# Optimization experiments

Hardware: AMD Instinct MI355X
Metric: run time of the kernel (lower is better)

Reference implementation:

```python
import jax, jax.numpy as jnp
import numpy as np

B, S, D_MODEL, N_HEADS, D_HEAD = 2, 2048, 512, 8, 64
AMBIENT_K = -1.0
EPS = 1e-7


def log_map_origin(x, K):
    """Lorentz log map at origin, curvature K<0. x: (..., d+1) -> (..., d)."""
    c = -K
    sc = jnp.sqrt(c)
    x_t = x[..., :1]
    x_s = x[..., 1:]
    nrm = jnp.maximum(jnp.linalg.norm(x_s, axis=-1, keepdims=True), EPS)
    theta = jnp.arccosh(jnp.maximum(sc * x_t, 1.0 + EPS)) / sc  # geodesic distance
    return theta * x_s / nrm


def exp_map_batched(u, K_vals):
    """Per-head Lorentz exp map at origin. u: (B,S,H,dh), K_vals: (H,) negative.
    Returns (B,S,H,dh+1) with time component first."""
    c = (-K_vals)[None, None, :, None]          # (1,1,H,1)
    sc = jnp.sqrt(c)
    n = jnp.maximum(jnp.linalg.norm(u, axis=-1, keepdims=True), EPS)
    t = jnp.cosh(sc * n) / sc                   # time component
    s = jnp.sinh(sc * n) / (sc * n) * u         # space components
    return jnp.concatenate([t, s], axis=-1)


def setup_inputs() -> dict:
    key = jax.random.key(0)
    k_x, k_q, k_k, k_v, k_o = jax.random.split(key, 5)
    # Lorentz points on the K=-1 manifold: x_t = sqrt(1 + |x_s|^2)
    x_s = 0.5 * jax.random.normal(k_x, (B, S, D_MODEL), dtype=jnp.float32)
    x_t = jnp.sqrt(1.0 + jnp.sum(x_s * x_s, axis=-1, keepdims=True))
    x = jnp.concatenate([x_t, x_s], axis=-1)    # (B, S, d_model+1)
    scale = 1.0 / np.sqrt(D_MODEL)
    W_q = scale * jax.random.normal(k_q, (D_MODEL, N_HEADS * D_HEAD), dtype=jnp.float32)
    W_k = scale * jax.random.normal(k_k, (D_MODEL, N_HEADS * D_HEAD), dtype=jnp.float32)
    W_v = scale * jax.random.normal(k_v, (D_MODEL, N_HEADS * D_HEAD), dtype=jnp.float32)
    W_o = scale * jax.random.normal(k_o, (N_HEADS * D_HEAD, D_MODEL), dtype=jnp.float32)
    log_abs_K = jnp.zeros((N_HEADS,), dtype=jnp.float32)  # init_K = -1 -> log(1) = 0
    return {"x": x, "W_q": W_q, "W_k": W_k, "W_v": W_v, "W_o": W_o,
            "log_abs_K": log_abs_K}


def reference(x, W_q, W_k, W_v, W_o, log_abs_K):
    b, s, _ = x.shape
    K_vals = -jnp.exp(log_abs_K)                            # (H,) negative curvatures
    x_eu = log_map_origin(x, AMBIENT_K)                     # (B,S,D)
    Q = (x_eu @ W_q).reshape(b, s, N_HEADS, D_HEAD)
    Kp = (x_eu @ W_k).reshape(b, s, N_HEADS, D_HEAD)
    V = (x_eu @ W_v).reshape(b, s, N_HEADS, D_HEAD)
    Q_hyp = exp_map_batched(Q, K_vals).transpose(0, 2, 1, 3)   # (B,H,S,dh+1)
    K_hyp = exp_map_batched(Kp, K_vals).transpose(0, 2, 1, 3)
    V = V.transpose(0, 2, 1, 3)                                # (B,H,S,dh)
    Q_t, Q_s = Q_hyp[..., 0], Q_hyp[..., 1:]
    K_t, K_s = K_hyp[..., 0], K_hyp[..., 1:]
    # Lorentzian inner product: -q_t k_t + <q_s, k_s>
    lorentz_ip = (jnp.einsum('bhqd,bhkd->bhqk', Q_s, K_s)
                  - jnp.einsum('bhq,bhk->bhqk', Q_t, K_t))
    abs_K = jnp.exp(log_abs_K)[None, :, None, None]
    scores = abs_K * (-lorentz_ip) / np.sqrt(D_HEAD)           # (B,H,S,S)
    causal = jnp.triu(jnp.ones((s, s), dtype=bool), k=1)[None, None]
    scores = jnp.where(causal, -jnp.inf, scores)
    attn = jax.nn.softmax(scores, axis=-1)
    out = jnp.einsum('bhqk,bhkd->bhqd', attn, V)               # (B,H,S,dh)
    out = out.transpose(0, 2, 1, 3).reshape(b, s, N_HEADS * D_HEAD)
    return out @ W_o                                           # (B,S,D)
```

## Files before the change

kernel.cpp:

```cpp
#include <hip/hip_runtime.h>
#include <math.h>

#define S_LEN 2048
#define B_SZ 2
#define NH 8
#define DH 64
#define DM 512
#define MROWS 4096

typedef __attribute__((ext_vector_type(8))) short s16x8;
typedef __attribute__((ext_vector_type(4))) float fx4;
typedef __attribute__((ext_vector_type(16))) float fx16;
typedef __attribute__((ext_vector_type(4))) int ix4;

__device__ inline short f2bf(float x){
  unsigned u = __float_as_uint(x);
  u = (u + 0x7FFFu + ((u >> 16) & 1u)) >> 16;
  return (short)u;
}

__device__ inline fx4 mfma16(s16x8 a, s16x8 b, fx4 c){
  return __builtin_amdgcn_mfma_f32_16x16x32_bf16(a, b, c, 0, 0, 0);
}
__device__ inline fx16 mfma32(s16x8 a, s16x8 b, fx16 c){
  return __builtin_amdgcn_mfma_f32_32x32x16_bf16(a, b, c, 0, 0, 0);
}
__device__ inline int cvtpk(float a, float b){
  int r; asm("v_cvt_pk_bf16_f32 %0, %1, %2" : "=v"(r) : "v"(a), "v"(b)); return r;
}

#define GLL16(g, l) __builtin_amdgcn_global_load_lds((const __attribute__((address_space(1))) void*)(g), (__attribute__((address_space(3))) void*)(l), 16, 0, 0)
#define GLL4(g, l)  __builtin_amdgcn_global_load_lds((const __attribute__((address_space(1))) void*)(g), (__attribute__((address_space(3))) void*)(l), 4, 0, 0)

__global__ __launch_bounds__(256) void prep_kernel(const float* __restrict__ W0,
                                                   const float* __restrict__ W1,
                                                   const float* __restrict__ W2,
                                                   const float* __restrict__ W3,
                                                   short* __restrict__ Wt,
                                                   const float* __restrict__ x,
                                                   short* __restrict__ xeu){
  __shared__ short tile[64][66];
  __shared__ float s4[4];
  int bid = blockIdx.x;
  int t = threadIdx.x;
  if (bid < 256){
    int z = bid >> 6, rem = bid & 63;
    const float* W = (z == 0) ? W0 : (z == 1) ? W1 : (z == 2) ? W2 : W3;
    short* Wtz = Wt + (size_t)z * DM * DM;
    int n0 = (rem & 7) * 64, k0 = (rem >> 3) * 64;
    int nl = t & 63;
    #pragma unroll
    for (int p = 0; p < 16; ++p){
      int kl = (t >> 6) + p * 4;
      tile[kl][nl] = f2bf(W[(size_t)(k0 + kl) * DM + n0 + nl]);
    }
    __syncthreads();
    int kl2 = t & 63;
    #pragma unroll
    for (int p = 0; p < 16; ++p){
      int nl2 = (t >> 6) + p * 4;
      Wtz[(size_t)(n0 + nl2) * DM + k0 + kl2] = tile[kl2][nl2];
    }
  } else {
    int row = 2 * (bid - 256) + (t >> 7);
    int tl = t & 127;
    const float* xr = x + (size_t)row * (DM + 1);
    float v[4]; float ss = 0.f;
    #pragma unroll
    for (int j = 0; j < 4; ++j){
      v[j] = xr[1 + tl + 128 * j];
      ss += v[j] * v[j];
    }
    #pragma unroll
    for (int off = 1; off < 64; off <<= 1) ss += __shfl_xor(ss, off);
    if ((t & 63) == 0) s4[t >> 6] = ss;
    __syncthreads();
    int g2 = t >> 7;
    float tot = s4[2 * g2] + s4[2 * g2 + 1];
    float nrm = sqrtf(tot);
    float xt = xr[0];
    float theta = acoshf(fmaxf(xt, 1.0f + 1e-7f));
    float scl = theta / fmaxf(nrm, 1e-7f);
    #pragma unroll
    for (int j = 0; j < 4; ++j)
      xeu[(size_t)row * DM + tl + 128 * j] = f2bf(scl * v[j]);
  }
}

__global__ __launch_bounds__(256, 3) void gemm_fused_kernel(const short* __restrict__ A,
                                                            const short* __restrict__ Bt,
                                                            const float* __restrict__ labsK,
                                                            float* __restrict__ Qt,
                                                            short* __restrict__ Qs,
                                                            float* __restrict__ Kt,
                                                            short* __restrict__ Ks,
                                                            short* __restrict__ Vt){
  __shared__ __attribute__((aligned(16))) short Asm[2][128 * 64];
  __shared__ __attribute__((aligned(16))) short Bsm[2][64 * 64];
  __shared__ float nrm2s[2][128];
  const int K = DM;
  int z = blockIdx.z;
  int h = blockIdx.x;
  int n0 = h * 64, m0 = blockIdx.y * 128;
  int t = threadIdx.x;
  int w = t >> 6, lane = t & 63;
  int wm = w >> 1, wn = w & 1;
  int lg = lane >> 4, lr = lane & 15;
  const short* Btz = Bt + (size_t)z * K * DM;

  int aoff[4]; const short* asrcp[4];
  int boff[2]; const short* bsrcp[2];
  #pragma unroll
  for (int j = 0; j < 4; ++j){
    int ch = t + 256 * j;
    int r = ch >> 3, c = ch & 7;
    aoff[j] = ch * 8;
    asrcp[j] = A + (size_t)(m0 + r) * K + 8 * (c ^ (r & 7));
  }
  #pragma unroll
  for (int j = 0; j < 2; ++j){
    int ch = t + 256 * j;
    int r = ch >> 3, c = ch & 7;
    boff[j] = ch * 8;
    bsrcp[j] = Btz + (size_t)(n0 + r) * K + 8 * (c ^ (r & 7));
  }

  {
    short* ab = &Asm[0][0]; short* bb = &Bsm[0][0];
    #pragma unroll
    for (int j = 0; j < 4; ++j) GLL16(asrcp[j], ab + aoff[j]);
    #pragma unroll
    for (int j = 0; j < 2; ++j) GLL16(bsrcp[j], bb + boff[j]);
  }

  fx4 acc[4][2] = {};
  int buf = 0;
  for (int ks = 0; ks < 8; ++ks){
    if (ks < 7){
      int nb = buf ^ 1;
      short* ab = &Asm[nb][0]; short* bb = &Bsm[nb][0];
      int kk = (ks + 1) * 64;
      #pragma unroll
      for (int j = 0; j < 4; ++j) GLL16(asrcp[j] + kk, ab + aoff[j]);
      #pragma unroll
      for (int j = 0; j < 2; ++j) GLL16(bsrcp[j] + kk, bb + boff[j]);
      asm volatile("s_waitcnt vmcnt(6)" ::: "memory");
    } else {
      asm volatile("s_waitcnt vmcnt(0)" ::: "memory");
    }
    __builtin_amdgcn_s_barrier();

    s16x8 af[4][2], bf[2][2];
    #pragma unroll
    for (int mi = 0; mi < 4; ++mi){
      int row = wm * 64 + mi * 16 + lr;
      #pragma unroll
      for (int s = 0; s < 2; ++s)
        af[mi][s] = *(const s16x8*)&Asm[buf][row * 64 + ((4 * s + lg) ^ (row & 7)) * 8];
    }
    #pragma unroll
    for (int ni = 0; ni < 2; ++ni){
      int row = wn * 32 + ni * 16 + lr;
      #pragma unroll
      for (int s = 0; s < 2; ++s)
        bf[ni][s] = *(const s16x8*)&Bsm[buf][row * 64 + ((4 * s + lg) ^ (row & 7)) * 8];
    }
    #pragma unroll
    for (int s = 0; s < 2; ++s)
      #pragma unroll
      for (int mi = 0; mi < 4; ++mi)
        #pragma unroll
        for (int ni = 0; ni < 2; ++ni)
          acc[mi][ni] = mfma16(af[mi][s], bf[ni][s], acc[mi][ni]);
    __builtin_amdgcn_s_barrier();
    buf ^= 1;
  }

  if (z < 2){
    #pragma unroll
    for (int mi = 0; mi < 4; ++mi)
      #pragma unroll
      for (int r = 0; r < 4; ++r){
        float prt = acc[mi][0][r] * acc[mi][0][r] + acc[mi][1][r] * acc[mi][1][r];
        prt += __shfl_xor(prt, 1);
        prt += __shfl_xor(prt, 2);
        prt += __shfl_xor(prt, 4);
        prt += __shfl_xor(prt, 8);
        if (lr == 0) nrm2s[wn][wm * 64 + mi * 16 + 4 * lg + r] = prt;
      }
    __syncthreads();
    float c  = __expf(labsK[h]);
    float sc = sqrtf(c);
    float invsc = __frcp_rn(sc);
    float a  = 0.125f * c * 1.4426950408889634f;
    float tmul = (z == 0) ? a : 1.0f;
    float vmul = (z == 0) ? -a : 1.0f;
    float* Tt = (z == 0) ? Qt : Kt;
    short* Ts = (z == 0) ? Qs : Ks;
    #pragma unroll
    for (int mi = 0; mi < 4; ++mi)
      #pragma unroll
      for (int r = 0; r < 4; ++r){
        int row_local = wm * 64 + mi * 16 + 4 * lg + r;
        float full = nrm2s[0][row_local] + nrm2s[1][row_local];
        float n = fmaxf(sqrtf(full), 1e-7f);
        float arg = sc * n;
        float e = __expf(arg), ei = __frcp_rn(e);
        float tval = tmul * 0.5f * (e + ei) * invsc;
        float vscl = vmul * 0.5f * (e - ei) * __frcp_rn(arg);
        int grow = m0 + row_local;
        int b = grow >> 11, s = grow & (S_LEN - 1);
        size_t bhs = ((size_t)(b * NH + h) * S_LEN + s);
        if (lr == 0) Tt[bhs] = tval;
        #pragma unroll
        for (int ni = 0; ni < 2; ++ni)
          Ts[bhs * DH + wn * 32 + ni * 16 + lr] = f2bf(vscl * acc[mi][ni][r]);
      }
  } else {
    short* vt = (short*)&Asm[0][0];
    #pragma unroll
    for (int mi = 0; mi < 4; ++mi)
      #pragma unroll
      for (int ni = 0; ni < 2; ++ni)
        #pragma unroll
        for (int r = 0; r < 4; ++r){
          int row_local = wm * 64 + mi * 16 + 4 * lg + r;
          int col_local = wn * 32 + ni * 16 + lr;
          vt[col_local * 136 + row_local] = f2bf(acc[mi][ni][r]);
        }
    __syncthreads();
    int d = t >> 2, sseg = (t & 3) * 32;
    int b = m0 >> 11;
    size_t vbase = ((size_t)(b * NH + h) * DH + d) * S_LEN + (m0 & (S_LEN - 1)) + sseg;
    #pragma unroll
    for (int j = 0; j < 4; ++j){
      s16x8 val = *(const s16x8*)&vt[d * 136 + sseg + 8 * j];
      *(s16x8*)(Vt + vbase + 8 * j) = val;
    }
  }
}

__global__ __launch_bounds__(256, 4) void attn_kernel(const short* __restrict__ Qs,
                                                      const float* __restrict__ Qt,
                                                      const short* __restrict__ Ks,
                                                      const float* __restrict__ Kt,
                                                      const short* __restrict__ Vt,
                                                      float* __restrict__ Mpart,
                                                      float* __restrict__ Lpart,
                                                      float* __restrict__ Opart){
  __shared__ __attribute__((aligned(16))) short Ksm[2][4096];
  __shared__ __attribute__((aligned(16))) short Vsm[2][4096];
  __shared__ __attribute__((aligned(16))) float Ktm[2][64];

  int bx = blockIdx.x;
  int bh = bx & 15;
  int id = bx >> 4;
  int g, c;
  if (id < 4)       { g = id;                 c = 0; }
  else if (id < 12) { g = 4 + ((id - 4) >> 1);  c = (id - 4) & 1; }
  else if (id < 24) { int r = id - 12; int q3 = r / 3; g = 8 + q3; c = r - 3 * q3; }
  else              { g = 12 + ((id - 24) >> 2); c = (id - 24) & 3; }
  int kbeg = 512 * c;
  int kend = 512 * c + 512; { int ge = 128 * g + 128; if (ge < kend) kend = ge; }
  int ntc = (kend - kbeg) >> 6;

  int tid = threadIdx.x;
  int w = tid >> 6, lane = tid & 63;
  int l5 = lane & 31, hi = lane >> 5;
  size_t bhS = (size_t)bh * S_LEN;

  const short* Kg  = Ks + bhS * DH;
  const short* Vg  = Vt + (size_t)bh * DH * S_LEN;
  const float* Ktg = Kt + bhS;

  int srow = lane >> 3;
  int scol = ((lane & 7) * 8) ^ (srow << 3);
  const short* kg0 = Kg + (size_t)(kbeg + 16 * w + srow) * DH + scol;
  const short* kg1 = kg0 + 8 * DH;
  const short* vg0 = Vg + (size_t)(16 * w + srow) * S_LEN + kbeg + scol;
  const short* vg1 = vg0 + 8 * S_LEN;
  const float* ktg = Ktg + kbeg + lane;
  short* Kd0 = &Ksm[0][16 * w * 64]; short* Kd1 = Kd0 + 512;
  short* Vd0 = &Vsm[0][16 * w * 64]; short* Vd1 = Vd0 + 512;

  int q0w = 128 * g + 32 * w;
  int q   = q0w + l5;
  int qmax = q0w + 31;
  s16x8 qf[4];
  #pragma unroll
  for (int dblk = 0; dblk < 4; ++dblk)
    qf[dblk] = *(const s16x8*)(Qs + (bhS + q) * DH + dblk * 16 + hi * 8);
  float aqt = Qt[bhS + q];

  fx16 acc0, acc1;
  #pragma unroll
  for (int i = 0; i < 16; ++i){ acc0[i] = 0.f; acc1[i] = 0.f; }
  float mrun = 0.f, lrun = 0.f;

  GLL16(kg0, Kd0); GLL16(kg1, Kd1);
  GLL16(vg0, Vd0); GLL16(vg1, Vd1);
  if (w == 3) GLL4(ktg, &Ktm[0][0]);
  int buf = 0;

  for (int t = 0; t < ntc; ++t){
    int k0 = kbeg + t * 64;
    if (t + 1 < ntc){
      int off = (t + 1) * 64;
      int bn = buf ^ 1;
      GLL16(kg0 + (size_t)off * DH, &Ksm[bn][16 * w * 64]);
      GLL16(kg1 + (size_t)off * DH, &Ksm[bn][16 * w * 64 + 512]);
      GLL16(vg0 + off, &Vsm[bn][16 * w * 64]);
      GLL16(vg1 + off, &Vsm[bn][16 * w * 64 + 512]);
      if (w == 3){
        GLL4(ktg + off, &Ktm[bn][0]);
        asm volatile("s_waitcnt vmcnt(5)" ::: "memory");
      } else {
        asm volatile("s_waitcnt vmcnt(4)" ::: "memory");
      }
    } else {
      asm volatile("s_waitcnt vmcnt(0)" ::: "memory");
    }
    __builtin_amdgcn_s_barrier();

    if (k0 <= qmax){
      fx16 st[2];
      __builtin_amdgcn_s_setprio(1);
      #pragma unroll
      for (int s = 0; s < 2; ++s){
        const short* kb = &Ksm[buf][(32 * s + l5) * 64];
        fx16 z;
        #pragma unroll
        for (int i = 0; i < 16; ++i) z[i] = 0.f;
        #pragma unroll
        for (int dblk = 0; dblk < 4; ++dblk){
          s16x8 kf = *(const s16x8*)(kb + ((16 * dblk + 8 * hi) ^ ((l5 & 7) << 3)));
          z = mfma32(kf, qf[dblk], z);
        }
        st[s] = z;
      }
      __builtin_amdgcn_s_setprio(0);
      float p[2][16];
      #pragma unroll
      for (int s = 0; s < 2; ++s)
        #pragma unroll
        for (int m4 = 0; m4 < 4; ++m4){
          fx4 kt4 = *(const fx4*)&Ktm[buf][32 * s + 8 * m4 + 4 * hi];
          #pragma unroll
          for (int tt = 0; tt < 4; ++tt)
            p[s][4 * m4 + tt] = st[s][4 * m4 + tt] + aqt * kt4[tt];
        }
      if (k0 + 63 > q0w){
        #pragma unroll
        for (int s = 0; s < 2; ++s)
          #pragma unroll
          for (int r = 0; r < 16; ++r){
            int kg2 = k0 + 32 * s + (r & 3) + 8 * (r >> 2) + 4 * hi;
            if (kg2 > q) p[s][r] = -3e38f;
          }
      }
      float v16[16];
      #pragma unroll
      for (int i = 0; i < 16; ++i) v16[i] = fmaxf(p[0][i], p[1][i]);
      #pragma unroll
      for (int i = 0; i < 8; ++i) v16[i] = fmaxf(v16[i], v16[i + 8]);
      #pragma unroll
      for (int i = 0; i < 4; ++i) v16[i] = fmaxf(v16[i], v16[i + 4]);
      float pmax = fmaxf(fmaxf(v16[0], v16[1]), fmaxf(v16[2], v16[3]));
      pmax = fmaxf(pmax, __shfl_xor(pmax, 32));
      if (!__all(pmax <= mrun + 8.f)){
        float mnew = fmaxf(mrun, pmax);
        float scl = __builtin_amdgcn_exp2f(mrun - mnew);
        mrun = mnew;
        lrun *= scl;
        #pragma unroll
        for (int i = 0; i < 16; ++i){ acc0[i] *= scl; acc1[i] *= scl; }
      }
      float sm[16];
      #pragma unroll
      for (int i = 0; i < 16; ++i){
        p[0][i] = __builtin_amdgcn_exp2f(p[0][i] - mrun);
        p[1][i] = __builtin_amdgcn_exp2f(p[1][i] - mrun);
        sm[i] = p[0][i] + p[1][i];
      }
      #pragma unroll
      for (int i = 0; i < 8; ++i) sm[i] += sm[i + 8];
      #pragma unroll
      for (int i = 0; i < 4; ++i) sm[i] += sm[i + 4];
      float rsum = (sm[0] + sm[1]) + (sm[2] + sm[3]);
      rsum += __shfl_xor(rsum, 32);
      lrun += rsum;

      #pragma unroll
      for (int h = 0; h < 4; ++h){
        int s = h >> 1, hb = h & 1;
        int w0 = cvtpk(p[s][8 * hb + 0], p[s][8 * hb + 1]);
        int w1 = cvtpk(p[s][8 * hb + 2], p[s][8 * hb + 3]);
        int w2 = cvtpk(p[s][8 * hb + 4], p[s][8 * hb + 5]);
        int w3 = cvtpk(p[s][8 * hb + 6], p[s][8 * hb + 7]);
        int sdA = hi ? w0 : w2;
        int sdB = hi ? w1 : w3;
        int rcA = __shfl_xor(sdA, 32);
        int rcB = __shfl_xor(sdB, 32);
        ix4 fw;
        fw.x = hi ? rcA : w0; fw.y = hi ? rcB : w1;
        fw.z = hi ? w2 : rcA; fw.w = hi ? w3 : rcB;
        s16x8 pf = __builtin_bit_cast(s16x8, fw);
        const short* vb0 = &Vsm[buf][(l5) * 64 + ((16 * h + 8 * hi) ^ ((l5 & 7) << 3))];
        const short* vb1 = vb0 + 32 * 64;
        s16x8 vf0 = *(const s16x8*)vb0;
        s16x8 vf1 = *(const s16x8*)vb1;
        __builtin_amdgcn_s_setprio(1);
        acc0 = mfma32(vf0, pf, acc0);
        acc1 = mfma32(vf1, pf, acc1);
        __builtin_amdgcn_s_setprio(0);
      }
    }
    __builtin_amdgcn_s_barrier();
    buf ^= 1;
  }

  int slot = bh * 40 + id;
  if (hi == 0){
    Mpart[(size_t)slot * 128 + 32 * w + l5] = mrun;
    Lpart[(size_t)slot * 128 + 32 * w + l5] = lrun;
  }
  float* Op = Opart + (size_t)slot * 8192 + w * 2048;
  #pragma unroll
  for (int r = 0; r < 16; ++r){
    int d = (r & 3) + 8 * (r >> 2) + 4 * hi;
    Op[d * 32 + l5]        = acc0[r];
    Op[(d + 32) * 32 + l5] = acc1[r];
  }
}

__global__ __launch_bounds__(256) void combine_kernel(const float* __restrict__ Mpart,
                                                      const float* __restrict__ Lpart,
                                                      const float* __restrict__ Opart,
                                                      short* __restrict__ Obf){
  int bx = blockIdx.x;
  int bhg = bx & 255;
  int bh = bhg & 15, g = bhg >> 4;
  int t = threadIdx.x;
  int q = t & 127;
  int dquad = (t >> 7) | ((bx >> 8) << 1);
  int nch = (g >> 2) + 1;
  int pre = (g < 4) ? g : (g < 8 ? 4 + 2 * (g - 4) : (g < 12 ? 12 + 3 * (g - 8) : 24 + 4 * (g - 12)));
  int base = bh * 40 + pre;
  int w = q >> 5, l = q & 31;

  float mc[4], lc[4];
  #pragma unroll
  for (int c = 0; c < 4; ++c){
    mc[c] = Mpart[(size_t)(base + c) * 128 + q];
    lc[c] = Lpart[(size_t)(base + c) * 128 + q];
    if (c >= nch) mc[c] = -3e38f;
  }
  float M = fmaxf(fmaxf(mc[0], mc[1]), fmaxf(mc[2], mc[3]));
  float wc[4]; float L = 0.f;
  #pragma unroll
  for (int c = 0; c < 4; ++c){
    wc[c] = __builtin_amdgcn_exp2f(mc[c] - M);
    L += wc[c] * lc[c];
  }
  float invL = 1.f / L;
  #pragma unroll
  for (int c = 0; c < 4; ++c) wc[c] *= invL;

  const float* ob = Opart + (size_t)base * 8192 + w * 2048 + dquad * 256 + l;
  float f[4][8];
  #pragma unroll
  for (int c = 0; c < 4; ++c)
    #pragma unroll
    for (int dd = 0; dd < 8; ++dd)
      f[c][dd] = ob[(size_t)c * 8192 + dd * 32];
  s16x8 pk;
  #pragma unroll
  for (int dd = 0; dd < 8; ++dd){
    float o = wc[0] * f[0][dd] + wc[1] * f[1][dd] + wc[2] * f[2][dd] + wc[3] * f[3][dd];
    pk[dd] = f2bf(o);
  }
  int bb = bh >> 3, hh = bh & 7;
  *(s16x8*)(Obf + ((size_t)bb * S_LEN + 128 * g + q) * DM + hh * DH + dquad * 8) = pk;
}

__global__ __launch_bounds__(256, 4) void gemm_o_kernel(const short* __restrict__ A,
                                                        const short* __restrict__ Bt,
                                                        float* __restrict__ C){
  __shared__ __attribute__((aligned(16))) short Asm[2][64 * 64];
  __shared__ __attribute__((aligned(16))) short Bsm[2][64 * 64];
  const int K = DM;
  int n0 = blockIdx.x * 64, m0 = blockIdx.y * 64;
  int t = threadIdx.x;
  int w = t >> 6, lane = t & 63;
  int wm = w >> 1, wn = w & 1;
  int lg = lane >> 4, lr = lane & 15;

  int aoff[2]; const short* asrcp[2];
  int boff[2]; const short* bsrcp[2];
  #pragma unroll
  for (int j = 0; j < 2; ++j){
    int ch = t + 256 * j;
    int r = ch >> 3, c = ch & 7;
    aoff[j] = ch * 8;
    asrcp[j] = A + (size_t)(m0 + r) * K + 8 * (c ^ (r & 7));
    boff[j] = ch * 8;
    bsrcp[j] = Bt + (size_t)(n0 + r) * K + 8 * (c ^ (r & 7));
  }

  {
    short* ab = &Asm[0][0]; short* bb = &Bsm[0][0];
    #pragma unroll
    for (int j = 0; j < 2; ++j){ GLL16(asrcp[j], ab + aoff[j]); GLL16(bsrcp[j], bb + boff[j]); }
  }

  fx4 acc[2][2] = {};
  int buf = 0;
  for (int ks = 0; ks < 8; ++ks){
    if (ks < 7){
      int nb = buf ^ 1;
      short* ab = &Asm[nb][0]; short* bb = &Bsm[nb][0];
      int kk = (ks + 1) * 64;
      #pragma unroll
      for (int j = 0; j < 2; ++j){ GLL16(asrcp[j] + kk, ab + aoff[j]); GLL16(bsrcp[j] + kk, bb + boff[j]); }
      asm volatile("s_waitcnt vmcnt(4)" ::: "memory");
    } else {
      asm volatile("s_waitcnt vmcnt(0)" ::: "memory");
    }
    __builtin_amdgcn_s_barrier();

    s16x8 af[2][2], bf[2][2];
    #pragma unroll
    for (int mi = 0; mi < 2; ++mi){
      int row = wm * 32 + mi * 16 + lr;
      #pragma unroll
      for (int s = 0; s < 2; ++s)
        af[mi][s] = *(const s16x8*)&Asm[buf][row * 64 + ((4 * s + lg) ^ (row & 7)) * 8];
    }
    #pragma unroll
    for (int ni = 0; ni < 2; ++ni){
      int row = wn * 32 + ni * 16 + lr;
      #pragma unroll
      for (int s = 0; s < 2; ++s)
        bf[ni][s] = *(const s16x8*)&Bsm[buf][row * 64 + ((4 * s + lg) ^ (row & 7)) * 8];
    }
    #pragma unroll
    for (int s = 0; s < 2; ++s)
      #pragma unroll
      for (int mi = 0; mi < 2; ++mi)
        #pragma unroll
        for (int ni = 0; ni < 2; ++ni)
          acc[mi][ni] = mfma16(af[mi][s], bf[ni][s], acc[mi][ni]);
    __builtin_amdgcn_s_barrier();
    buf ^= 1;
  }

  #pragma unroll
  for (int mi = 0; mi < 2; ++mi)
    #pragma unroll
    for (int ni = 0; ni < 2; ++ni)
      #pragma unroll
      for (int r = 0; r < 4; ++r){
        int row = m0 + wm * 32 + mi * 16 + 4 * lg + r;
        int col = n0 + wn * 32 + ni * 16 + lr;
        C[(size_t)row * DM + col] = acc[mi][ni][r];
      }
}

extern "C" void kernel_launch(void* const* d_in, const int* in_sizes, int n_in,
                              void* d_out, int out_size, void* d_ws, size_t ws_size,
                              hipStream_t stream) {
  const float* x     = (const float*)d_in[0];
  const float* Wq    = (const float*)d_in[1];
  const float* Wk    = (const float*)d_in[2];
  const float* Wv    = (const float*)d_in[3];
  const float* Wo    = (const float*)d_in[4];
  const float* labsK = (const float*)d_in[5];

  char* w = (char*)d_ws;
  short* Wt    = (short*)(w);
  short* xeu   = (short*)(w + (2ull  << 20));
  float* Opart = (float*)(w + (6ull  << 20));
  float* Mpart = (float*)(w + (26ull << 20));
  float* Lpart = (float*)(w + (27ull << 20));
  short* Qs    = (short*)(w + (30ull << 20));
  short* Ks    = (short*)(w + (34ull << 20));
  short* Vt    = (short*)(w + (38ull << 20));
  float* Qt    = (float*)(w + (42ull << 20));
  float* Kt    = (float*)(w + (42ull << 20) + (128ull << 10));
  short* Obf   = (short*)(w + (42ull << 20) + (256ull << 10));

  prep_kernel<<<dim3(2304), 256, 0, stream>>>(Wq, Wk, Wv, Wo, Wt, x, xeu);

  gemm_fused_kernel<<<dim3(8, 32, 3), 256, 0, stream>>>(
      xeu, Wt, labsK, Qt, Qs, Kt, Ks, Vt);

  attn_kernel<<<dim3(640), 256, 0, stream>>>(Qs, Qt, Ks, Kt, Vt, Mpart, Lpart, Opart);

  combine_kernel<<<dim3(1024), 256, 0, stream>>>(Mpart, Lpart, Opart, Obf);

  gemm_o_kernel<<<dim3(8, 64), 256, 0, stream>>>(Obf, Wt + 3 * DM * DM, (float*)d_out);
}
```

Baseline: 66.28 us.

## Fuse split-K combine into attention via atomic counter, triple-buffer K/V, reorder GEMM grids

The separate combine kernel is removed. The last attention block per (bh, query group) detects completion through an atomic counter and performs the split-K softmax merge, writing bf16 output directly. Attention K/V staging becomes triple-buffered with prefetch two tiles ahead, occupancy drops to 3 blocks per SM, and the Opart layout changes to per-query rows for vector stores. The GEMM kernels swap grid axes, move the wait and barrier to the loop top, and raise wave priority around the MFMAs. This adds a memset launch and fence/atomic overhead in exchange for one fewer kernel launch.

```diff
diff --git a/kernel.cpp b/kernel.cpp
--- a/kernel.cpp
+++ b/kernel.cpp
@@ -100,8 +100,8 @@
   __shared__ float nrm2s[2][128];
   const int K = DM;
   int z = blockIdx.z;
-  int h = blockIdx.x;
-  int n0 = h * 64, m0 = blockIdx.y * 128;
+  int h = blockIdx.y;
+  int n0 = h * 64, m0 = blockIdx.x * 128;
   int t = threadIdx.x;
   int w = t >> 6, lane = t & 63;
   int wm = w >> 1, wn = w & 1;
@@ -134,22 +134,19 @@
   }
 
   fx4 acc[4][2] = {};
-  int buf = 0;
   for (int ks = 0; ks < 8; ++ks){
+    asm volatile("s_waitcnt vmcnt(0)" ::: "memory");
+    __builtin_amdgcn_s_barrier();
     if (ks < 7){
-      int nb = buf ^ 1;
+      int nb = (ks + 1) & 1;
       short* ab = &Asm[nb][0]; short* bb = &Bsm[nb][0];
       int kk = (ks + 1) * 64;
       #pragma unroll
       for (int j = 0; j < 4; ++j) GLL16(asrcp[j] + kk, ab + aoff[j]);
       #pragma unroll
       for (int j = 0; j < 2; ++j) GLL16(bsrcp[j] + kk, bb + boff[j]);
-      asm volatile("s_waitcnt vmcnt(6)" ::: "memory");
-    } else {
-      asm volatile("s_waitcnt vmcnt(0)" ::: "memory");
-    }
-    __builtin_amdgcn_s_barrier();
-
+    }
+    int buf = ks & 1;
     s16x8 af[4][2], bf[2][2];
     #pragma unroll
     for (int mi = 0; mi < 4; ++mi){
@@ -165,6 +162,7 @@
       for (int s = 0; s < 2; ++s)
         bf[ni][s] = *(const s16x8*)&Bsm[buf][row * 64 + ((4 * s + lg) ^ (row & 7)) * 8];
     }
+    __builtin_amdgcn_s_setprio(1);
     #pragma unroll
     for (int s = 0; s < 2; ++s)
       #pragma unroll
@@ -172,8 +170,7 @@
         #pragma unroll
         for (int ni = 0; ni < 2; ++ni)
           acc[mi][ni] = mfma16(af[mi][s], bf[ni][s], acc[mi][ni]);
-    __builtin_amdgcn_s_barrier();
-    buf ^= 1;
+    __builtin_amdgcn_s_setprio(0);
   }
 
   if (z < 2){
@@ -218,6 +215,7 @@
       }
   } else {
     short* vt = (short*)&Asm[0][0];
+    __syncthreads();
     #pragma unroll
     for (int mi = 0; mi < 4; ++mi)
       #pragma unroll
@@ -240,17 +238,20 @@
   }
 }
 
-__global__ __launch_bounds__(256, 4) void attn_kernel(const short* __restrict__ Qs,
+__global__ __launch_bounds__(256, 3) void attn_kernel(const short* __restrict__ Qs,
                                                       const float* __restrict__ Qt,
                                                       const short* __restrict__ Ks,
                                                       const float* __restrict__ Kt,
                                                       const short* __restrict__ Vt,
                                                       float* __restrict__ Mpart,
                                                       float* __restrict__ Lpart,
-                                                      float* __restrict__ Opart){
-  __shared__ __attribute__((aligned(16))) short Ksm[2][4096];
-  __shared__ __attribute__((aligned(16))) short Vsm[2][4096];
-  __shared__ __attribute__((aligned(16))) float Ktm[2][64];
+                                                      float* __restrict__ Opart,
+                                                      int* __restrict__ cnt,
+                                                      short* __restrict__ Obf){
+  __shared__ __attribute__((aligned(16))) short Ksm[3][4096];
+  __shared__ __attribute__((aligned(16))) short Vsm[3][4096];
+  __shared__ __attribute__((aligned(16))) float Ktm[3][64];
+  __shared__ int lastFlag;
 
   int bx = blockIdx.x;
   int bh = bx & 15;
@@ -260,6 +261,7 @@
   else if (id < 12) { g = 4 + ((id - 4) >> 1);  c = (id - 4) & 1; }
   else if (id < 24) { int r = id - 12; int q3 = r / 3; g = 8 + q3; c = r - 3 * q3; }
   else              { g = 12 + ((id - 24) >> 2); c = (id - 24) & 3; }
+  int nch = (g >> 2) + 1;
   int kbeg = 512 * c;
   int kend = 512 * c + 512; { int ge = 128 * g + 128; if (ge < kend) kend = ge; }
   int ntc = (kend - kbeg) >> 6;
@@ -280,8 +282,6 @@
   const short* vg0 = Vg + (size_t)(16 * w + srow) * S_LEN + kbeg + scol;
   const short* vg1 = vg0 + 8 * S_LEN;
   const float* ktg = Ktg + kbeg + lane;
-  short* Kd0 = &Ksm[0][16 * w * 64]; short* Kd1 = Kd0 + 512;
-  short* Vd0 = &Vsm[0][16 * w * 64]; short* Vd1 = Vd0 + 512;
 
   int q0w = 128 * g + 32 * w;
   int q   = q0w + l5;
@@ -297,30 +297,27 @@
   for (int i = 0; i < 16; ++i){ acc0[i] = 0.f; acc1[i] = 0.f; }
   float mrun = 0.f, lrun = 0.f;
 
-  GLL16(kg0, Kd0); GLL16(kg1, Kd1);
-  GLL16(vg0, Vd0); GLL16(vg1, Vd1);
-  if (w == 3) GLL4(ktg, &Ktm[0][0]);
-  int buf = 0;
-
+  #define STAGE_T(tt, b) { int off_ = (tt) * 64; \
+    GLL16(kg0 + (size_t)off_ * DH, &Ksm[b][16 * w * 64]); \
+    GLL16(kg1 + (size_t)off_ * DH, &Ksm[b][16 * w * 64 + 512]); \
+    GLL16(vg0 + off_, &Vsm[b][16 * w * 64]); \
+    GLL16(vg1 + off_, &Vsm[b][16 * w * 64 + 512]); \
+    if (w == 3) GLL4(ktg + off_, &Ktm[b][0]); }
+
+  STAGE_T(0, 0);
+  if (ntc > 1) STAGE_T(1, 1);
+
+  int buf = 0, sbuf = 2;
   for (int t = 0; t < ntc; ++t){
     int k0 = kbeg + t * 64;
     if (t + 1 < ntc){
-      int off = (t + 1) * 64;
-      int bn = buf ^ 1;
-      GLL16(kg0 + (size_t)off * DH, &Ksm[bn][16 * w * 64]);
-      GLL16(kg1 + (size_t)off * DH, &Ksm[bn][16 * w * 64 + 512]);
-      GLL16(vg0 + off, &Vsm[bn][16 * w * 64]);
-      GLL16(vg1 + off, &Vsm[bn][16 * w * 64 + 512]);
-      if (w == 3){
-        GLL4(ktg + off, &Ktm[bn][0]);
-        asm volatile("s_waitcnt vmcnt(5)" ::: "memory");
-      } else {
-        asm volatile("s_waitcnt vmcnt(4)" ::: "memory");
-      }
+      if (w == 3) asm volatile("s_waitcnt vmcnt(5)" ::: "memory");
+      else        asm volatile("s_waitcnt vmcnt(4)" ::: "memory");
     } else {
       asm volatile("s_waitcnt vmcnt(0)" ::: "memory");
     }
     __builtin_amdgcn_s_barrier();
+    if (t + 2 < ntc) STAGE_T(t + 2, sbuf);
 
     if (k0 <= qmax){
       fx16 st[2];
@@ -415,72 +412,75 @@
         __builtin_amdgcn_s_setprio(0);
       }
     }
-    __builtin_amdgcn_s_barrier();
-    buf ^= 1;
-  }
-
-  int slot = bh * 40 + id;
+    buf  = (buf == 2)  ? 0 : buf + 1;
+    sbuf = (sbuf == 2) ? 0 : sbuf + 1;
+  }
+
+  int slot = ((bh << 4) + g) * 4 + c;
+  int qi = 32 * w + l5;
   if (hi == 0){
-    Mpart[(size_t)slot * 128 + 32 * w + l5] = mrun;
-    Lpart[(size_t)slot * 128 + 32 * w + l5] = lrun;
-  }
-  float* Op = Opart + (size_t)slot * 8192 + w * 2048;
+    Mpart[(size_t)slot * 128 + qi] = mrun;
+    Lpart[(size_t)slot * 128 + qi] = lrun;
+  }
+  float* Op = Opart + (size_t)slot * 8192 + (size_t)qi * 64;
   #pragma unroll
-  for (int r = 0; r < 16; ++r){
-    int d = (r & 3) + 8 * (r >> 2) + 4 * hi;
-    Op[d * 32 + l5]        = acc0[r];
-    Op[(d + 32) * 32 + l5] = acc1[r];
-  }
-}
-
-__global__ __launch_bounds__(256) void combine_kernel(const float* __restrict__ Mpart,
-                                                      const float* __restrict__ Lpart,
-                                                      const float* __restrict__ Opart,
-                                                      short* __restrict__ Obf){
-  int bx = blockIdx.x;
-  int bhg = bx & 255;
-  int bh = bhg & 15, g = bhg >> 4;
-  int t = threadIdx.x;
-  int q = t & 127;
-  int dquad = (t >> 7) | ((bx >> 8) << 1);
-  int nch = (g >> 2) + 1;
-  int pre = (g < 4) ? g : (g < 8 ? 4 + 2 * (g - 4) : (g < 12 ? 12 + 3 * (g - 8) : 24 + 4 * (g - 12)));
-  int base = bh * 40 + pre;
-  int w = q >> 5, l = q & 31;
-
-  float mc[4], lc[4];
-  #pragma unroll
-  for (int c = 0; c < 4; ++c){
-    mc[c] = Mpart[(size_t)(base + c) * 128 + q];
-    lc[c] = Lpart[(size_t)(base + c) * 128 + q];
-    if (c >= nch) mc[c] = -3e38f;
-  }
-  float M = fmaxf(fmaxf(mc[0], mc[1]), fmaxf(mc[2], mc[3]));
-  float wc[4]; float L = 0.f;
-  #pragma unroll
-  for (int c = 0; c < 4; ++c){
-    wc[c] = __builtin_amdgcn_exp2f(mc[c] - M);
-    L += wc[c] * lc[c];
-  }
-  float invL = 1.f / L;
-  #pragma unroll
-  for (int c = 0; c < 4; ++c) wc[c] *= invL;
-
-  const float* ob = Opart + (size_t)base * 8192 + w * 2048 + dquad * 256 + l;
-  float f[4][8];
-  #pragma unroll
-  for (int c = 0; c < 4; ++c)
-    #pragma unroll
-    for (int dd = 0; dd < 8; ++dd)
-      f[c][dd] = ob[(size_t)c * 8192 + dd * 32];
-  s16x8 pk;
-  #pragma unroll
-  for (int dd = 0; dd < 8; ++dd){
-    float o = wc[0] * f[0][dd] + wc[1] * f[1][dd] + wc[2] * f[2][dd] + wc[3] * f[3][dd];
-    pk[dd] = f2bf(o);
-  }
-  int bb = bh >> 3, hh = bh & 7;
-  *(s16x8*)(Obf + ((size_t)bb * S_LEN + 128 * g + q) * DM + hh * DH + dquad * 8) = pk;
+  for (int j = 0; j < 4; ++j){
+    fx4 v0, v1;
+    #pragma unroll
+    for (int i = 0; i < 4; ++i){ v0[i] = acc0[4 * j + i]; v1[i] = acc1[4 * j + i]; }
+    *(fx4*)(Op + 8 * j + 4 * hi)      = v0;
+    *(fx4*)(Op + 32 + 8 * j + 4 * hi) = v1;
+  }
+
+  __threadfence();
+  if (tid == 0){
+    int old = __hip_atomic_fetch_add(&cnt[(bh << 4) + g], 1,
+                                     __ATOMIC_ACQ_REL, __HIP_MEMORY_SCOPE_AGENT);
+    lastFlag = (old == nch - 1);
+  }
+  __syncthreads();
+  if (lastFlag){
+    __threadfence();
+    int qf2 = tid & 127;
+    int oct0 = tid >> 7;
+    int gbase = ((bh << 4) + g) * 4;
+    float mc[4], lc[4];
+    #pragma unroll
+    for (int cc = 0; cc < 4; ++cc){
+      mc[cc] = Mpart[(size_t)(gbase + cc) * 128 + qf2];
+      lc[cc] = Lpart[(size_t)(gbase + cc) * 128 + qf2];
+      if (cc >= nch) mc[cc] = -3e38f;
+    }
+    float M = fmaxf(fmaxf(mc[0], mc[1]), fmaxf(mc[2], mc[3]));
+    float wc[4]; float L = 0.f;
+    #pragma unroll
+    for (int cc = 0; cc < 4; ++cc){
+      wc[cc] = __builtin_amdgcn_exp2f(mc[cc] - M);
+      L += wc[cc] * lc[cc];
+    }
+    float invL = 1.f / L;
+    #pragma unroll
+    for (int cc = 0; cc < 4; ++cc) wc[cc] *= invL;
+    int bb = bh >> 3, hh = bh & 7;
+    short* orow = Obf + ((size_t)bb * S_LEN + 128 * g + qf2) * DM + hh * DH;
+    const float* obase = Opart + (size_t)gbase * 8192 + (size_t)qf2 * 64;
+    #pragma unroll
+    for (int i = 0; i < 4; ++i){
+      int oct = oct0 + 2 * i;
+      float accf[8] = {0.f,0.f,0.f,0.f,0.f,0.f,0.f,0.f};
+      #pragma unroll
+      for (int cc = 0; cc < 4; ++cc){
+        fx4 a = *(const fx4*)(obase + (size_t)cc * 8192 + oct * 8);
+        fx4 b = *(const fx4*)(obase + (size_t)cc * 8192 + oct * 8 + 4);
+        #pragma unroll
+        for (int k = 0; k < 4; ++k){ accf[k] += wc[cc] * a[k]; accf[4 + k] += wc[cc] * b[k]; }
+      }
+      s16x8 pk;
+      #pragma unroll
+      for (int dd = 0; dd < 8; ++dd) pk[dd] = f2bf(accf[dd]);
+      *(s16x8*)(orow + oct * 8) = pk;
+    }
+  }
 }
 
 __global__ __launch_bounds__(256, 4) void gemm_o_kernel(const short* __restrict__ A,
@@ -489,7 +489,7 @@
   __shared__ __attribute__((aligned(16))) short Asm[2][64 * 64];
   __shared__ __attribute__((aligned(16))) short Bsm[2][64 * 64];
   const int K = DM;
-  int n0 = blockIdx.x * 64, m0 = blockIdx.y * 64;
+  int n0 = blockIdx.y * 64, m0 = blockIdx.x * 64;
   int t = threadIdx.x;
   int w = t >> 6, lane = t & 63;
   int wm = w >> 1, wn = w & 1;
@@ -514,20 +514,17 @@
   }
 
   fx4 acc[2][2] = {};
-  int buf = 0;
   for (int ks = 0; ks < 8; ++ks){
+    asm volatile("s_waitcnt vmcnt(0)" ::: "memory");
+    __builtin_amdgcn_s_barrier();
     if (ks < 7){
-      int nb = buf ^ 1;
+      int nb = (ks + 1) & 1;
       short* ab = &Asm[nb][0]; short* bb = &Bsm[nb][0];
       int kk = (ks + 1) * 64;
       #pragma unroll
       for (int j = 0; j < 2; ++j){ GLL16(asrcp[j] + kk, ab + aoff[j]); GLL16(bsrcp[j] + kk, bb + boff[j]); }
-      asm volatile("s_waitcnt vmcnt(4)" ::: "memory");
-    } else {
-      asm volatile("s_waitcnt vmcnt(0)" ::: "memory");
-    }
-    __builtin_amdgcn_s_barrier();
-
+    }
+    int buf = ks & 1;
     s16x8 af[2][2], bf[2][2];
     #pragma unroll
     for (int mi = 0; mi < 2; ++mi){
@@ -543,6 +540,7 @@
       for (int s = 0; s < 2; ++s)
         bf[ni][s] = *(const s16x8*)&Bsm[buf][row * 64 + ((4 * s + lg) ^ (row & 7)) * 8];
     }
+    __builtin_amdgcn_s_setprio(1);
     #pragma unroll
     for (int s = 0; s < 2; ++s)
       #pragma unroll
@@ -550,8 +548,7 @@
         #pragma unroll
         for (int ni = 0; ni < 2; ++ni)
           acc[mi][ni] = mfma16(af[mi][s], bf[ni][s], acc[mi][ni]);
-    __builtin_amdgcn_s_barrier();
-    buf ^= 1;
+    __builtin_amdgcn_s_setprio(0);
   }
 
   #pragma unroll
@@ -579,24 +576,26 @@
   char* w = (char*)d_ws;
   short* Wt    = (short*)(w);
   short* xeu   = (short*)(w + (2ull  << 20));
-  float* Opart = (float*)(w + (6ull  << 20));
-  float* Mpart = (float*)(w + (26ull << 20));
-  float* Lpart = (float*)(w + (27ull << 20));
   short* Qs    = (short*)(w + (30ull << 20));
   short* Ks    = (short*)(w + (34ull << 20));
   short* Vt    = (short*)(w + (38ull << 20));
   float* Qt    = (float*)(w + (42ull << 20));
   float* Kt    = (float*)(w + (42ull << 20) + (128ull << 10));
   short* Obf   = (short*)(w + (42ull << 20) + (256ull << 10));
+  float* Opart = (float*)(w + (48ull << 20));
+  float* Mpart = (float*)(w + (80ull << 20));
+  float* Lpart = (float*)(w + (81ull << 20));
+  int*   cnt   = (int*)  (w + (82ull << 20));
+
+  hipMemsetAsync(cnt, 0, 256 * sizeof(int), stream);
 
   prep_kernel<<<dim3(2304), 256, 0, stream>>>(Wq, Wk, Wv, Wo, Wt, x, xeu);
 
-  gemm_fused_kernel<<<dim3(8, 32, 3), 256, 0, stream>>>(
+  gemm_fused_kernel<<<dim3(32, 8, 3), 256, 0, stream>>>(
       xeu, Wt, labsK, Qt, Qs, Kt, Ks, Vt);
 
-  attn_kernel<<<dim3(640), 256, 0, stream>>>(Qs, Qt, Ks, Kt, Vt, Mpart, Lpart, Opart);
-
-  combine_kernel<<<dim3(1024), 256, 0, stream>>>(Mpart, Lpart, Opart, Obf);
-
-  gemm_o_kernel<<<dim3(8, 64), 256, 0, stream>>>(Obf, Wt + 3 * DM * DM, (float*)d_out);
-}
+  attn_kernel<<<dim3(640), 256, 0, stream>>>(
+      Qs, Qt, Ks, Kt, Vt, Mpart, Lpart, Opart, cnt, Obf);
+
+  gemm_o_kernel<<<dim3(64, 8), 256, 0, stream>>>(Obf, Wt + 3 * DM * DM, (float*)d_out);
+}
```

Result: slower. 216.0 us (+225.9%).
